# Performance work log

Hardware: AMD Instinct MI355X
Metric: run time of the kernel (lower is better)

## Reference

```python
import jax, jax.numpy as jnp
from jax import lax
import numpy as np

N_HEADS = 8
TANH_CLIP = 10.0
NEG = -1e9  # grad-safe stand-in for -inf mask value


def setup_inputs() -> dict:
    key = jax.random.key(0)
    k0, k1, k2, k3, k4 = jax.random.split(key, 5)
    B, N, D = 256, 512, 128
    s = 1.0 / np.sqrt(D)
    embeddings = jax.random.normal(k0, (B, N, D), jnp.float32)
    W_node = jax.random.normal(k1, (D, 3 * D), jnp.float32) * s   # project_node_embeddings
    W_fixed = jax.random.normal(k2, (D, D), jnp.float32) * s      # project_fixed_context
    W_step = jax.random.normal(k3, (D + 1, D), jnp.float32) * s   # project_step_context (D+1 input)
    W_out = jax.random.normal(k4, (D, D), jnp.float32) * s        # project_out
    return {"embeddings": embeddings, "W_node": W_node, "W_fixed": W_fixed,
            "W_step": W_step, "W_out": W_out, "num_steps": 64}


def reference(embeddings, W_node, W_fixed, W_step, W_out, num_steps):
    B, N, D = embeddings.shape
    H = N_HEADS
    dk = D // H
    dt = embeddings.dtype

    # ---- _precompute: fixed context, cached per-head keys/values, logit key ----
    graph_embed = embeddings.mean(axis=1)                     # [B, D]
    fixed_ctx = graph_embed @ W_fixed                         # [B, D]
    proj = embeddings @ W_node                                # [B, N, 3D]
    gK, gV, logitK = jnp.split(proj, 3, axis=-1)              # each [B, N, D]
    Kh = gK.reshape(B, N, H, dk).transpose(2, 0, 1, 3)        # [H, B, N, dk]
    Vh = gV.reshape(B, N, H, dk).transpose(2, 0, 1, 3)        # [H, B, N, dk]

    inv_sqrt_dk = jnp.asarray(1.0 / np.sqrt(dk), dt)
    inv_sqrt_d = jnp.asarray(1.0 / np.sqrt(D), dt)
    fracs = jnp.arange(num_steps, dtype=dt) / num_steps       # step-context scalar feature
    batch_idx = jnp.arange(B)

    def step(carry, frac):
        visited, current = carry                              # [B, N] bool, [B] int32
        # step context: current node embedding + scalar (remaining-fraction analogue)
        cur_emb = jnp.take_along_axis(embeddings, current[:, None, None], axis=1)[:, 0, :]
        step_ctx = jnp.concatenate([cur_emb, jnp.full((B, 1), frac, dt)], axis=-1)
        q = fixed_ctx + step_ctx @ W_step                     # [B, D] glimpse query
        Qh = q.reshape(B, H, dk).transpose(1, 0, 2)           # [H, B, dk]
        # glimpse attention with inner masking
        compat = jnp.einsum('hbd,hbnd->hbn', Qh, Kh) * inv_sqrt_dk
        compat = jnp.where(visited[None, :, :], NEG, compat)  # mask_inner
        attn = jax.nn.softmax(compat, axis=-1)
        heads = jnp.einsum('hbn,hbnd->hbd', attn, Vh)         # [H, B, dk]
        glimpse = heads.transpose(1, 0, 2).reshape(B, D) @ W_out
        # single-head tanh-clipped logits against logit key
        logits = jnp.einsum('bd,bnd->bn', glimpse, logitK) * inv_sqrt_d
        logits = jnp.tanh(logits) * TANH_CLIP
        logits = jnp.where(visited, NEG, logits)              # mask_logits
        log_p = jax.nn.log_softmax(logits, axis=-1)           # [B, N]
        selected = jnp.argmax(log_p, axis=-1).astype(jnp.int32)  # greedy decode
        visited = visited.at[batch_idx, selected].set(True)
        return (visited, selected), (log_p, selected)

    visited0 = jnp.zeros((B, N), bool)
    current0 = jnp.zeros((B,), jnp.int32)
    _, (log_ps, seqs) = lax.scan(step, (visited0, current0), fracs)
    return log_ps.transpose(1, 0, 2), seqs.transpose(1, 0)   # [B, T, N], [B, T]
```

## Files before the change

### kernel.cpp

```cpp
#include <hip/hip_runtime.h>

#define BB 256
#define NN 512
#define DD 128
#define HH 8

static constexpr float NEGC = -1e9f;
static constexpr float INV_SQRT_D = 0.08838834764831845f;

__device__ __forceinline__ float dot4(float4 a, float4 b) {
    return a.x * b.x + a.y * b.y + a.z * b.z + a.w * b.w;
}
__device__ __forceinline__ void fma4(float4& a, float p, float4 e) {
    a.x += p * e.x; a.y += p * e.y; a.z += p * e.z; a.w += p * e.w;
}

__global__ __launch_bounds__(128)
void precompute_fc(const float* __restrict__ E, const float* __restrict__ Wf,
                   float* __restrict__ fc) {
    int b = blockIdx.x, d = threadIdx.x;
    __shared__ float ge[DD];
    const float* Eb = E + (size_t)b * NN * DD;
    float s = 0.f;
    for (int n = 0; n < NN; ++n) s += Eb[n * DD + d];
    ge[d] = s * (1.0f / 512.0f);
    __syncthreads();
    float o = 0.f;
    for (int k = 0; k < DD; ++k) o += ge[k] * Wf[k * DD + d];
    fc[b * DD + d] = o;
}

__global__ __launch_bounds__(128)
void precompute_w(const float* __restrict__ Wn, const float* __restrict__ Wout,
                  float* __restrict__ Wog, float* __restrict__ WkT) {
    int k = blockIdx.x, d = threadIdx.x;
    WkT[k * DD + d] = Wn[d * 384 + k];
    float s = 0.f;
    for (int e = 0; e < DD; ++e) s += Wout[k * DD + e] * Wn[d * 384 + 256 + e];
    Wog[k * DD + d] = s;
}

struct SMw12 {
    float EA[NN * 64];
    float Pt[NN * 8];
    float qt[HH * DD];
    float qarr[DD];
    float fcs[DD];
    float hcv[DD];
    float gs[DD];
    float curE[DD];
    float l[HH];
    float Mh[HH];
    float redf[16];
    float stat[2];
    unsigned char visf[NN];
    int   cur;
    float rbv;
};

__global__ __launch_bounds__(512)
void decoder(const float* __restrict__ E, const float* __restrict__ Ws,
             const float* __restrict__ Wn, const float* __restrict__ fc,
             const float* __restrict__ Wog, const float* __restrict__ WkT,
             float* __restrict__ out_logp, float* __restrict__ out_seq, int T) {
    __shared__ SMw12 sm;
    const int b = blockIdx.x, tid = threadIdx.x;
    const int lane = tid & 63, wv = tid >> 6;
    const int g4 = tid >> 7, d128 = tid & 127;
    const float* Eg = E + (size_t)b * NN * DD;
    const float4* Ef4 = (const float4*)Eg;

    float* const slots = &sm.Pt[0];
    float* const part  = &sm.Pt[0];
    float* const lgp   = &sm.Pt[512];
    float* const ebp   = &sm.qt[0];

    #pragma unroll
    for (int i = 0; i < 16; ++i) {
        int f = i * 512 + tid;
        int nn = f >> 4, cq = f & 15;
        *(float4*)&sm.EA[nn * 64 + ((cq ^ (nn & 15)) << 2)] = Ef4[nn * 32 + cq];
    }
    if (tid < DD) {
        sm.fcs[tid] = fc[b * DD + tid];
        sm.curE[tid] = Eg[tid];
    }
    sm.visf[tid] = 0;
    if (tid == 0) sm.cur = 0;
    {
        float s = 0.f;
        #pragma unroll 8
        for (int i = 0; i < 32; ++i) { float4 v = Ef4[tid * 32 + i]; s += dot4(v, v); }
        for (int o = 1; o < 64; o <<= 1) s = fmaxf(s, __shfl_xor(s, o));
        if (lane == 0) sm.redf[wv] = s;
    }
    __syncthreads();
    if (tid == 0) {
        float m = sm.redf[0];
        for (int i = 1; i < 8; ++i) m = fmaxf(m, sm.redf[i]);
        sm.rbv = sqrtf(m);
    }
    __syncthreads();

    for (int t = 0; t < T; ++t) {
        {
            float s = 0.f;
            const float* Wsg = Ws + d128;
            int k0 = g4 * 32;
            #pragma unroll 8
            for (int k = k0; k < k0 + 32; ++k) s += sm.curE[k] * Wsg[k * DD];
            if (g4 == 3) s += ((float)t / (float)T) * Wsg[DD * DD];
            part[g4 * 128 + d128] = s;
        }
        __syncthreads();
        if (tid < DD)
            sm.qarr[tid] = sm.fcs[tid] + part[0 * 128 + tid] + part[1 * 128 + tid]
                         + part[2 * 128 + tid] + part[3 * 128 + tid];
        __syncthreads();
        {
            const int hA = g4, hB = g4 + 4;
            const float* WA = WkT + (hA * 16) * DD + d128;
            const float* WB = WkT + (hB * 16) * DD + d128;
            float a = 0.f, c = 0.f;
            #pragma unroll
            for (int j = 0; j < 16; ++j) {
                a += sm.qarr[hA * 16 + j] * WA[j * DD];
                c += sm.qarr[hB * 16 + j] * WB[j * DD];
            }
            a *= 0.25f; c *= 0.25f;
            sm.qt[hA * DD + d128] = a;
            sm.qt[hB * DD + d128] = c;
            float sa = a * a, sc = c * c;
            for (int o = 1; o < 64; o <<= 1) {
                sa += __shfl_xor(sa, o);
                sc += __shfl_xor(sc, o);
            }
            if (lane == 0) { sm.redf[wv] = sa; sm.redf[8 + wv] = sc; }
        }
        __syncthreads();
        if (tid < 8) {
            int h = tid;
            float ss = (h < 4) ? (sm.redf[2 * h] + sm.redf[2 * h + 1])
                               : (sm.redf[8 + 2 * (h - 4)] + sm.redf[8 + 2 * (h - 4) + 1]);
            sm.Mh[h] = sqrtf(ss) * sm.rbv;
        }
        __syncthreads();

        if (tid < 256) {
            const int n0 = tid, n1 = tid + 256;
            const int m0 = n0 & 15, m1 = n1 & 15;
            float b0 = 0.f, b1 = 0.f, b2 = 0.f, b3 = 0.f,
                  b4 = 0.f, b5 = 0.f, b6 = 0.f, b7 = 0.f;
            float c0 = 0.f, c1 = 0.f, c2 = 0.f, c3 = 0.f,
                  c4 = 0.f, c5 = 0.f, c6 = 0.f, c7 = 0.f;
            #pragma unroll 4
            for (int qd = 0; qd < 16; ++qd) {
                float4 e0 = *(const float4*)&sm.EA[n0 * 64 + ((qd ^ m0) << 2)];
                float4 e1 = *(const float4*)&sm.EA[n1 * 64 + ((qd ^ m1) << 2)];
#define CH(h_, bb_, cc_) { float4 qv = *(const float4*)&sm.qt[h_ * DD + qd * 4]; \
                bb_ += dot4(qv, e0); cc_ += dot4(qv, e1); }
                CH(0, b0, c0) CH(1, b1, c1) CH(2, b2, c2) CH(3, b3, c3)
                CH(4, b4, c4) CH(5, b5, c5) CH(6, b6, c6) CH(7, b7, c7)
#undef CH
            }
            #pragma unroll 4
            for (int qd = 0; qd < 16; ++qd) {
                float4 e0 = Ef4[n0 * 32 + 16 + qd];
                float4 e1 = Ef4[n1 * 32 + 16 + qd];
#define CH(h_, bb_, cc_) { float4 qv = *(const float4*)&sm.qt[h_ * DD + 64 + qd * 4]; \
                bb_ += dot4(qv, e0); cc_ += dot4(qv, e1); }
                CH(0, b0, c0) CH(1, b1, c1) CH(2, b2, c2) CH(3, b3, c3)
                CH(4, b4, c4) CH(5, b5, c5) CH(6, b6, c6) CH(7, b7, c7)
#undef CH
            }
            const bool v0 = (sm.visf[n0] != 0), v1 = (sm.visf[n1] != 0);
            float4 P0a, P0b, P1a, P1b;
            P0a.x = v0 ? 0.f : expf(b0 - sm.Mh[0]);
            P0a.y = v0 ? 0.f : expf(b1 - sm.Mh[1]);
            P0a.z = v0 ? 0.f : expf(b2 - sm.Mh[2]);
            P0a.w = v0 ? 0.f : expf(b3 - sm.Mh[3]);
            P0b.x = v0 ? 0.f : expf(b4 - sm.Mh[4]);
            P0b.y = v0 ? 0.f : expf(b5 - sm.Mh[5]);
            P0b.z = v0 ? 0.f : expf(b6 - sm.Mh[6]);
            P0b.w = v0 ? 0.f : expf(b7 - sm.Mh[7]);
            P1a.x = v1 ? 0.f : expf(c0 - sm.Mh[0]);
            P1a.y = v1 ? 0.f : expf(c1 - sm.Mh[1]);
            P1a.z = v1 ? 0.f : expf(c2 - sm.Mh[2]);
            P1a.w = v1 ? 0.f : expf(c3 - sm.Mh[3]);
            P1b.x = v1 ? 0.f : expf(c4 - sm.Mh[4]);
            P1b.y = v1 ? 0.f : expf(c5 - sm.Mh[5]);
            P1b.z = v1 ? 0.f : expf(c6 - sm.Mh[6]);
            P1b.w = v1 ? 0.f : expf(c7 - sm.Mh[7]);
            *(float4*)&sm.Pt[n0 * 8]     = P0a;
            *(float4*)&sm.Pt[n0 * 8 + 4] = P0b;
            *(float4*)&sm.Pt[n1 * 8]     = P1a;
            *(float4*)&sm.Pt[n1 * 8 + 4] = P1b;
        }
        __syncthreads();

        {
            const int h = wv;
            float sl = 0.f;
            #pragma unroll
            for (int i = 0; i < 8; ++i) sl += sm.Pt[(lane + i * 64) * 8 + h];
            for (int o = 1; o < 64; o <<= 1) sl += __shfl_xor(sl, o);
            if (lane == 0) sm.l[h] = sl;
        }
        const int dq = tid & 31, ch = tid >> 5;
        float4 a0 = {0,0,0,0}, a1 = {0,0,0,0}, a2 = {0,0,0,0}, a3 = {0,0,0,0},
               a4 = {0,0,0,0}, a5 = {0,0,0,0}, a6 = {0,0,0,0}, a7 = {0,0,0,0};
        {
            const int r0 = ch * 32;
            #pragma unroll 2
            for (int i = 0; i < 32; ++i) {
                const int r = r0 + i;
                float4 ev = (dq < 16)
                    ? *(const float4*)&sm.EA[r * 64 + ((dq ^ (r & 15)) << 2)]
                    : Ef4[r * 32 + dq];
                float4 pA = *(const float4*)&sm.Pt[r * 8];
                float4 pB = *(const float4*)&sm.Pt[r * 8 + 4];
                fma4(a0, pA.x, ev); fma4(a1, pA.y, ev);
                fma4(a2, pA.z, ev); fma4(a3, pA.w, ev);
                fma4(a4, pB.x, ev); fma4(a5, pB.y, ev);
                fma4(a6, pB.z, ev); fma4(a7, pB.w, ev);
            }
        }
        __syncthreads();
        {
            const int slot = ch & 3, rnd = ch >> 2;
            #pragma unroll
            for (int rr = 0; rr < 4; ++rr) {
                if (rnd == rr) {
                    float* sp = slots + (size_t)slot * 1024 + dq * 4;
                    if (rr == 0) {
#define STW(h_, av_) *(float4*)&sp[h_ * 128] = av_;
                        STW(0, a0) STW(1, a1) STW(2, a2) STW(3, a3)
                        STW(4, a4) STW(5, a5) STW(6, a6) STW(7, a7)
#undef STW
                    } else {
#define STA(h_, av_) { float4 tv = *(float4*)&sp[h_ * 128];                  \
                        tv.x += av_.x; tv.y += av_.y; tv.z += av_.z; tv.w += av_.w; \
                        *(float4*)&sp[h_ * 128] = tv; }
                        STA(0, a0) STA(1, a1) STA(2, a2) STA(3, a3)
                        STA(4, a4) STA(5, a5) STA(6, a6) STA(7, a7)
#undef STA
                    }
                }
                __syncthreads();
            }
        }
        {
            const int h = tid >> 6, d2 = (tid & 63) * 2;
            float inv = 1.0f / sm.l[h];
            #pragma unroll
            for (int r = 0; r < 2; ++r) {
                int d = d2 + r;
                float a = slots[0 * 1024 + h * 128 + d] + slots[1 * 1024 + h * 128 + d]
                        + slots[2 * 1024 + h * 128 + d] + slots[3 * 1024 + h * 128 + d];
                ebp[h * 128 + d] = a * inv;
            }
        }
        __syncthreads();

        {
            float s = 0.f;
            int k0 = g4 * 32;
            const int hh = d128 >> 4;
            const float* Wv = Wn + 128 + d128;
            #pragma unroll 8
            for (int d = k0; d < k0 + 32; ++d) s += ebp[hh * 128 + d] * Wv[d * 384];
            part[g4 * 128 + d128] = s;
        }
        __syncthreads();
        if (tid < DD)
            sm.hcv[tid] = part[0 * 128 + tid] + part[1 * 128 + tid]
                        + part[2 * 128 + tid] + part[3 * 128 + tid];
        __syncthreads();
        {
            float s = 0.f;
            int k0 = g4 * 32;
            #pragma unroll 8
            for (int k = k0; k < k0 + 32; ++k) s += sm.hcv[k] * Wog[k * DD + d128];
            part[g4 * 128 + d128] = s;
        }
        __syncthreads();
        if (tid < DD)
            sm.gs[tid] = (part[0 * 128 + tid] + part[1 * 128 + tid]
                        + part[2 * 128 + tid] + part[3 * 128 + tid]) * INV_SQRT_D;
        __syncthreads();

        {
            const int n = tid, nm = n & 15;
            float s = 0.f;
            #pragma unroll 4
            for (int qd = 0; qd < 16; ++qd) {
                float4 gq = *(const float4*)&sm.gs[qd * 4];
                float4 ev = *(const float4*)&sm.EA[n * 64 + ((qd ^ nm) << 2)];
                s += dot4(gq, ev);
            }
            #pragma unroll 4
            for (int qd = 0; qd < 16; ++qd) {
                float4 gq = *(const float4*)&sm.gs[64 + qd * 4];
                float4 ev = Ef4[n * 32 + 16 + qd];
                s += dot4(gq, ev);
            }
            lgp[n] = sm.visf[n] ? NEGC : 10.0f * tanhf(s);
        }
        __syncthreads();

        if (wv == 0) {
            float x0 = lgp[lane],       x1 = lgp[lane + 64],
                  x2 = lgp[lane + 128], x3 = lgp[lane + 192],
                  x4 = lgp[lane + 256], x5 = lgp[lane + 320],
                  x6 = lgp[lane + 384], x7 = lgp[lane + 448];
            float m = fmaxf(fmaxf(fmaxf(x0, x1), fmaxf(x2, x3)),
                            fmaxf(fmaxf(x4, x5), fmaxf(x6, x7)));
            for (int o = 1; o < 64; o <<= 1) m = fmaxf(m, __shfl_xor(m, o));
            float ssum = expf(x0 - m) + expf(x1 - m) + expf(x2 - m) + expf(x3 - m)
                       + expf(x4 - m) + expf(x5 - m) + expf(x6 - m) + expf(x7 - m);
            for (int o = 1; o < 64; o <<= 1) ssum += __shfl_xor(ssum, o);
            float lse = logf(ssum);
            float bv = (x0 - m) - lse; int bi = lane;
#define AMX(xi, ii) { float v_ = ((xi) - m) - lse; int i_ = (ii);           \
            if (v_ > bv) { bv = v_; bi = i_; } }
            AMX(x1, lane + 64)  AMX(x2, lane + 128) AMX(x3, lane + 192)
            AMX(x4, lane + 256) AMX(x5, lane + 320) AMX(x6, lane + 384)
            AMX(x7, lane + 448)
#undef AMX
            for (int o = 1; o < 64; o <<= 1) {
                float ov = __shfl_xor(bv, o);
                int   oi = __shfl_xor(bi, o);
                if (ov > bv || (ov == bv && oi < bi)) { bv = ov; bi = oi; }
            }
            if (lane == 0) {
                sm.stat[0] = m;
                sm.stat[1] = lse;
                sm.cur = bi;
                out_seq[(size_t)b * T + t] = (float)bi;
            }
        }
        __syncthreads();
        {
            float lp = (lgp[tid] - sm.stat[0]) - sm.stat[1];
            out_logp[((size_t)b * T + t) * NN + tid] = lp;
            const int cu = sm.cur;
            if (tid == cu) sm.visf[tid] = 1;
            if (tid < DD) {
                float vv;
                if (tid < 64)
                    vv = sm.EA[cu * 64 + ((((tid >> 2) ^ (cu & 15))) << 2) + (tid & 3)];
                else
                    vv = Eg[cu * DD + tid];
                sm.curE[tid] = vv;
            }
        }
        __syncthreads();
    }
}

extern "C" void kernel_launch(void* const* d_in, const int* in_sizes, int n_in,
                              void* d_out, int out_size, void* d_ws, size_t ws_size,
                              hipStream_t stream) {
    const float* E    = (const float*)d_in[0];
    const float* Wn   = (const float*)d_in[1];
    const float* Wf   = (const float*)d_in[2];
    const float* Ws   = (const float*)d_in[3];
    const float* Wout = (const float*)d_in[4];
    float* out = (float*)d_out;

    const int T = out_size / (BB * (NN + 1));

    float* fcp = (float*)d_ws;
    float* Wog = fcp + BB * DD;
    float* WkT = Wog + DD * DD;

    precompute_fc<<<BB, 128, 0, stream>>>(E, Wf, fcp);
    precompute_w<<<DD, 128, 0, stream>>>(Wn, Wout, Wog, WkT);
    decoder<<<BB, 512, 0, stream>>>(E, Ws, Wn, fcp, Wog, WkT,
                                    out, out + (size_t)BB * T * NN, T);
}
```

Baseline: 2.056 ms.

## Double decoder block to 1024 threads, splitting per-node dot products across thread pairs

Launches the decoder with 1024 threads per batch row instead of 512. The glimpse compat and logit dot products now split each node's 128-dim work across two threads (shared-memory half and global half), combined with a lane shuffle. The attention-value accumulation splits heads across half-waves so each thread holds 4 instead of 8 float4 accumulators. This aims to hide latency through more waves per block and lower register pressure, at the cost of padding the probability buffer and leaving half the threads idle in the small projection phases.

```diff
diff --git a/kernel.cpp b/kernel.cpp
--- a/kernel.cpp
+++ b/kernel.cpp
@@ -40,9 +40,9 @@
     Wog[k * DD + d] = s;
 }
 
-struct SMw12 {
+struct SMw15 {
     float EA[NN * 64];
-    float Pt[NN * 8];
+    float Pt[NN * 12];
     float qt[HH * DD];
     float qarr[DD];
     float fcs[DD];
@@ -58,26 +58,25 @@
     float rbv;
 };
 
-__global__ __launch_bounds__(512)
+__global__ __launch_bounds__(1024)
 void decoder(const float* __restrict__ E, const float* __restrict__ Ws,
              const float* __restrict__ Wn, const float* __restrict__ fc,
              const float* __restrict__ Wog, const float* __restrict__ WkT,
              float* __restrict__ out_logp, float* __restrict__ out_seq, int T) {
-    __shared__ SMw12 sm;
+    __shared__ SMw15 sm;
     const int b = blockIdx.x, tid = threadIdx.x;
     const int lane = tid & 63, wv = tid >> 6;
-    const int g4 = tid >> 7, d128 = tid & 127;
     const float* Eg = E + (size_t)b * NN * DD;
     const float4* Ef4 = (const float4*)Eg;
 
     float* const slots = &sm.Pt[0];
     float* const part  = &sm.Pt[0];
-    float* const lgp   = &sm.Pt[512];
+    float* const lgp   = &sm.Pt[4096];
     float* const ebp   = &sm.qt[0];
 
     #pragma unroll
-    for (int i = 0; i < 16; ++i) {
-        int f = i * 512 + tid;
+    for (int i = 0; i < 8; ++i) {
+        int f = i * 1024 + tid;
         int nn = f >> 4, cq = f & 15;
         *(float4*)&sm.EA[nn * 64 + ((cq ^ (nn & 15)) << 2)] = Ef4[nn * 32 + cq];
     }
@@ -85,9 +84,9 @@
         sm.fcs[tid] = fc[b * DD + tid];
         sm.curE[tid] = Eg[tid];
     }
-    sm.visf[tid] = 0;
+    if (tid < NN) sm.visf[tid] = 0;
     if (tid == 0) sm.cur = 0;
-    {
+    if (tid < NN) {
         float s = 0.f;
         #pragma unroll 8
         for (int i = 0; i < 32; ++i) { float4 v = Ef4[tid * 32 + i]; s += dot4(v, v); }
@@ -103,7 +102,8 @@
     __syncthreads();
 
     for (int t = 0; t < T; ++t) {
-        {
+        if (tid < 512) {
+            const int g4 = tid >> 7, d128 = tid & 127;
             float s = 0.f;
             const float* Wsg = Ws + d128;
             int k0 = g4 * 32;
@@ -117,7 +117,8 @@
             sm.qarr[tid] = sm.fcs[tid] + part[0 * 128 + tid] + part[1 * 128 + tid]
                          + part[2 * 128 + tid] + part[3 * 128 + tid];
         __syncthreads();
-        {
+        if (tid < 512) {
+            const int g4 = tid >> 7, d128 = tid & 127;
             const int hA = g4, hB = g4 + 4;
             const float* WA = WkT + (hA * 16) * DD + d128;
             const float* WB = WkT + (hB * 16) * DD + d128;
@@ -146,103 +147,98 @@
         }
         __syncthreads();
 
-        if (tid < 256) {
-            const int n0 = tid, n1 = tid + 256;
-            const int m0 = n0 & 15, m1 = n1 & 15;
-            float b0 = 0.f, b1 = 0.f, b2 = 0.f, b3 = 0.f,
-                  b4 = 0.f, b5 = 0.f, b6 = 0.f, b7 = 0.f;
-            float c0 = 0.f, c1 = 0.f, c2 = 0.f, c3 = 0.f,
-                  c4 = 0.f, c5 = 0.f, c6 = 0.f, c7 = 0.f;
-            #pragma unroll 4
-            for (int qd = 0; qd < 16; ++qd) {
-                float4 e0 = *(const float4*)&sm.EA[n0 * 64 + ((qd ^ m0) << 2)];
-                float4 e1 = *(const float4*)&sm.EA[n1 * 64 + ((qd ^ m1) << 2)];
-#define CH(h_, bb_, cc_) { float4 qv = *(const float4*)&sm.qt[h_ * DD + qd * 4]; \
-                bb_ += dot4(qv, e0); cc_ += dot4(qv, e1); }
-                CH(0, b0, c0) CH(1, b1, c1) CH(2, b2, c2) CH(3, b3, c3)
-                CH(4, b4, c4) CH(5, b5, c5) CH(6, b6, c6) CH(7, b7, c7)
-#undef CH
-            }
-            #pragma unroll 4
-            for (int qd = 0; qd < 16; ++qd) {
-                float4 e0 = Ef4[n0 * 32 + 16 + qd];
-                float4 e1 = Ef4[n1 * 32 + 16 + qd];
-#define CH(h_, bb_, cc_) { float4 qv = *(const float4*)&sm.qt[h_ * DD + 64 + qd * 4]; \
-                bb_ += dot4(qv, e0); cc_ += dot4(qv, e1); }
-                CH(0, b0, c0) CH(1, b1, c1) CH(2, b2, c2) CH(3, b3, c3)
-                CH(4, b4, c4) CH(5, b5, c5) CH(6, b6, c6) CH(7, b7, c7)
-#undef CH
-            }
-            const bool v0 = (sm.visf[n0] != 0), v1 = (sm.visf[n1] != 0);
-            float4 P0a, P0b, P1a, P1b;
-            P0a.x = v0 ? 0.f : expf(b0 - sm.Mh[0]);
-            P0a.y = v0 ? 0.f : expf(b1 - sm.Mh[1]);
-            P0a.z = v0 ? 0.f : expf(b2 - sm.Mh[2]);
-            P0a.w = v0 ? 0.f : expf(b3 - sm.Mh[3]);
-            P0b.x = v0 ? 0.f : expf(b4 - sm.Mh[4]);
-            P0b.y = v0 ? 0.f : expf(b5 - sm.Mh[5]);
-            P0b.z = v0 ? 0.f : expf(b6 - sm.Mh[6]);
-            P0b.w = v0 ? 0.f : expf(b7 - sm.Mh[7]);
-            P1a.x = v1 ? 0.f : expf(c0 - sm.Mh[0]);
-            P1a.y = v1 ? 0.f : expf(c1 - sm.Mh[1]);
-            P1a.z = v1 ? 0.f : expf(c2 - sm.Mh[2]);
-            P1a.w = v1 ? 0.f : expf(c3 - sm.Mh[3]);
-            P1b.x = v1 ? 0.f : expf(c4 - sm.Mh[4]);
-            P1b.y = v1 ? 0.f : expf(c5 - sm.Mh[5]);
-            P1b.z = v1 ? 0.f : expf(c6 - sm.Mh[6]);
-            P1b.w = v1 ? 0.f : expf(c7 - sm.Mh[7]);
-            *(float4*)&sm.Pt[n0 * 8]     = P0a;
-            *(float4*)&sm.Pt[n0 * 8 + 4] = P0b;
-            *(float4*)&sm.Pt[n1 * 8]     = P1a;
-            *(float4*)&sm.Pt[n1 * 8 + 4] = P1b;
-        }
-        __syncthreads();
-
         {
+            const int n2 = tid >> 1, hf = tid & 1;
+            float a0 = 0.f, a1 = 0.f, a2 = 0.f, a3 = 0.f,
+                  a4 = 0.f, a5 = 0.f, a6 = 0.f, a7 = 0.f;
+            if (hf == 0) {
+                const int nm = n2 & 15;
+                #pragma unroll 4
+                for (int q = 0; q < 16; ++q) {
+                    float4 ev = *(const float4*)&sm.EA[n2 * 64 + ((q ^ nm) << 2)];
+                    const int qb = q * 4;
+                    a0 += dot4(*(const float4*)&sm.qt[0 * DD + qb], ev);
+                    a1 += dot4(*(const float4*)&sm.qt[1 * DD + qb], ev);
+                    a2 += dot4(*(const float4*)&sm.qt[2 * DD + qb], ev);
+                    a3 += dot4(*(const float4*)&sm.qt[3 * DD + qb], ev);
+                    a4 += dot4(*(const float4*)&sm.qt[4 * DD + qb], ev);
+                    a5 += dot4(*(const float4*)&sm.qt[5 * DD + qb], ev);
+                    a6 += dot4(*(const float4*)&sm.qt[6 * DD + qb], ev);
+                    a7 += dot4(*(const float4*)&sm.qt[7 * DD + qb], ev);
+                }
+            } else {
+                #pragma unroll 4
+                for (int q = 0; q < 16; ++q) {
+                    float4 ev = Ef4[n2 * 32 + 16 + q];
+                    const int qb = 64 + q * 4;
+                    a0 += dot4(*(const float4*)&sm.qt[0 * DD + qb], ev);
+                    a1 += dot4(*(const float4*)&sm.qt[1 * DD + qb], ev);
+                    a2 += dot4(*(const float4*)&sm.qt[2 * DD + qb], ev);
+                    a3 += dot4(*(const float4*)&sm.qt[3 * DD + qb], ev);
+                    a4 += dot4(*(const float4*)&sm.qt[4 * DD + qb], ev);
+                    a5 += dot4(*(const float4*)&sm.qt[5 * DD + qb], ev);
+                    a6 += dot4(*(const float4*)&sm.qt[6 * DD + qb], ev);
+                    a7 += dot4(*(const float4*)&sm.qt[7 * DD + qb], ev);
+                }
+            }
+            a0 += __shfl_xor(a0, 1); a1 += __shfl_xor(a1, 1);
+            a2 += __shfl_xor(a2, 1); a3 += __shfl_xor(a3, 1);
+            a4 += __shfl_xor(a4, 1); a5 += __shfl_xor(a5, 1);
+            a6 += __shfl_xor(a6, 1); a7 += __shfl_xor(a7, 1);
+            if (hf == 0) {
+                const bool vn = (sm.visf[n2] != 0);
+                float4 Pa, Pb;
+                Pa.x = vn ? 0.f : expf(a0 - sm.Mh[0]);
+                Pa.y = vn ? 0.f : expf(a1 - sm.Mh[1]);
+                Pa.z = vn ? 0.f : expf(a2 - sm.Mh[2]);
+                Pa.w = vn ? 0.f : expf(a3 - sm.Mh[3]);
+                Pb.x = vn ? 0.f : expf(a4 - sm.Mh[4]);
+                Pb.y = vn ? 0.f : expf(a5 - sm.Mh[5]);
+                Pb.z = vn ? 0.f : expf(a6 - sm.Mh[6]);
+                Pb.w = vn ? 0.f : expf(a7 - sm.Mh[7]);
+                *(float4*)&sm.Pt[n2 * 12]     = Pa;
+                *(float4*)&sm.Pt[n2 * 12 + 4] = Pb;
+            }
+        }
+        __syncthreads();
+
+        if (wv < 8) {
             const int h = wv;
             float sl = 0.f;
             #pragma unroll
-            for (int i = 0; i < 8; ++i) sl += sm.Pt[(lane + i * 64) * 8 + h];
+            for (int i = 0; i < 8; ++i) sl += sm.Pt[(lane + i * 64) * 12 + h];
             for (int o = 1; o < 64; o <<= 1) sl += __shfl_xor(sl, o);
             if (lane == 0) sm.l[h] = sl;
         }
-        const int dq = tid & 31, ch = tid >> 5;
-        float4 a0 = {0,0,0,0}, a1 = {0,0,0,0}, a2 = {0,0,0,0}, a3 = {0,0,0,0},
-               a4 = {0,0,0,0}, a5 = {0,0,0,0}, a6 = {0,0,0,0}, a7 = {0,0,0,0};
         {
+            const int ch = wv, dq = lane & 31, hg = lane >> 5;
             const int r0 = ch * 32;
+            float4 a0 = {0,0,0,0}, a1 = {0,0,0,0}, a2 = {0,0,0,0}, a3 = {0,0,0,0};
             #pragma unroll 2
             for (int i = 0; i < 32; ++i) {
                 const int r = r0 + i;
                 float4 ev = (dq < 16)
                     ? *(const float4*)&sm.EA[r * 64 + ((dq ^ (r & 15)) << 2)]
                     : Ef4[r * 32 + dq];
-                float4 pA = *(const float4*)&sm.Pt[r * 8];
-                float4 pB = *(const float4*)&sm.Pt[r * 8 + 4];
-                fma4(a0, pA.x, ev); fma4(a1, pA.y, ev);
-                fma4(a2, pA.z, ev); fma4(a3, pA.w, ev);
-                fma4(a4, pB.x, ev); fma4(a5, pB.y, ev);
-                fma4(a6, pB.z, ev); fma4(a7, pB.w, ev);
-            }
-        }
-        __syncthreads();
-        {
+                float4 p = (hg == 0) ? *(const float4*)&sm.Pt[r * 12]
+                                     : *(const float4*)&sm.Pt[r * 12 + 4];
+                fma4(a0, p.x, ev); fma4(a1, p.y, ev);
+                fma4(a2, p.z, ev); fma4(a3, p.w, ev);
+            }
+            __syncthreads();
             const int slot = ch & 3, rnd = ch >> 2;
             #pragma unroll
             for (int rr = 0; rr < 4; ++rr) {
                 if (rnd == rr) {
-                    float* sp = slots + (size_t)slot * 1024 + dq * 4;
+                    float* sp = slots + (size_t)slot * 1024 + (size_t)hg * 512 + dq * 4;
                     if (rr == 0) {
-#define STW(h_, av_) *(float4*)&sp[h_ * 128] = av_;
-                        STW(0, a0) STW(1, a1) STW(2, a2) STW(3, a3)
-                        STW(4, a4) STW(5, a5) STW(6, a6) STW(7, a7)
-#undef STW
+                        *(float4*)&sp[0 * 128] = a0; *(float4*)&sp[1 * 128] = a1;
+                        *(float4*)&sp[2 * 128] = a2; *(float4*)&sp[3 * 128] = a3;
                     } else {
-#define STA(h_, av_) { float4 tv = *(float4*)&sp[h_ * 128];                  \
+#define STA(j_, av_) { float4 tv = *(float4*)&sp[j_ * 128];                      \
                         tv.x += av_.x; tv.y += av_.y; tv.z += av_.z; tv.w += av_.w; \
-                        *(float4*)&sp[h_ * 128] = tv; }
+                        *(float4*)&sp[j_ * 128] = tv; }
                         STA(0, a0) STA(1, a1) STA(2, a2) STA(3, a3)
-                        STA(4, a4) STA(5, a5) STA(6, a6) STA(7, a7)
 #undef STA
                     }
                 }
@@ -250,19 +246,15 @@
             }
         }
         {
-            const int h = tid >> 6, d2 = (tid & 63) * 2;
-            float inv = 1.0f / sm.l[h];
-            #pragma unroll
-            for (int r = 0; r < 2; ++r) {
-                int d = d2 + r;
-                float a = slots[0 * 1024 + h * 128 + d] + slots[1 * 1024 + h * 128 + d]
-                        + slots[2 * 1024 + h * 128 + d] + slots[3 * 1024 + h * 128 + d];
-                ebp[h * 128 + d] = a * inv;
-            }
-        }
-        __syncthreads();
-
-        {
+            const int h = tid >> 7, d = tid & 127;
+            float a = slots[0 * 1024 + h * 128 + d] + slots[1 * 1024 + h * 128 + d]
+                    + slots[2 * 1024 + h * 128 + d] + slots[3 * 1024 + h * 128 + d];
+            ebp[h * 128 + d] = a * (1.0f / sm.l[h]);
+        }
+        __syncthreads();
+
+        if (tid < 512) {
+            const int g4 = tid >> 7, d128 = tid & 127;
             float s = 0.f;
             int k0 = g4 * 32;
             const int hh = d128 >> 4;
@@ -276,7 +268,8 @@
             sm.hcv[tid] = part[0 * 128 + tid] + part[1 * 128 + tid]
                         + part[2 * 128 + tid] + part[3 * 128 + tid];
         __syncthreads();
-        {
+        if (tid < 512) {
+            const int g4 = tid >> 7, d128 = tid & 127;
             float s = 0.f;
             int k0 = g4 * 32;
             #pragma unroll 8
@@ -290,21 +283,24 @@
         __syncthreads();
 
         {
-            const int n = tid, nm = n & 15;
+            const int n2 = tid >> 1, hf = tid & 1;
             float s = 0.f;
-            #pragma unroll 4
-            for (int qd = 0; qd < 16; ++qd) {
-                float4 gq = *(const float4*)&sm.gs[qd * 4];
-                float4 ev = *(const float4*)&sm.EA[n * 64 + ((qd ^ nm) << 2)];
-                s += dot4(gq, ev);
-            }
-            #pragma unroll 4
-            for (int qd = 0; qd < 16; ++qd) {
-                float4 gq = *(const float4*)&sm.gs[64 + qd * 4];
-                float4 ev = Ef4[n * 32 + 16 + qd];
-                s += dot4(gq, ev);
-            }
-            lgp[n] = sm.visf[n] ? NEGC : 10.0f * tanhf(s);
+            if (hf == 0) {
+                const int nm = n2 & 15;
+                #pragma unroll 4
+                for (int q = 0; q < 16; ++q) {
+                    float4 ev = *(const float4*)&sm.EA[n2 * 64 + ((q ^ nm) << 2)];
+                    s += dot4(*(const float4*)&sm.gs[q * 4], ev);
+                }
+            } else {
+                #pragma unroll 4
+                for (int q = 0; q < 16; ++q) {
+                    float4 ev = Ef4[n2 * 32 + 16 + q];
+                    s += dot4(*(const float4*)&sm.gs[64 + q * 4], ev);
+                }
+            }
+            s += __shfl_xor(s, 1);
+            if (hf == 0) lgp[n2] = sm.visf[n2] ? NEGC : 10.0f * tanhf(s);
         }
         __syncthreads();
 
@@ -340,7 +336,7 @@
             }
         }
         __syncthreads();
-        {
+        if (tid < NN) {
             float lp = (lgp[tid] - sm.stat[0]) - sm.stat[1];
             out_logp[((size_t)b * T + t) * NN + tid] = lp;
             const int cu = sm.cur;
@@ -376,6 +372,6 @@
 
     precompute_fc<<<BB, 128, 0, stream>>>(E, Wf, fcp);
     precompute_w<<<DD, 128, 0, stream>>>(Wn, Wout, Wog, WkT);
-    decoder<<<BB, 512, 0, stream>>>(E, Ws, Wn, fcp, Wog, WkT,
-                                    out, out + (size_t)BB * T * NN, T);
-}
+    decoder<<<BB, 1024, 0, stream>>>(E, Ws, Wn, fcp, Wog, WkT,
+                                     out, out + (size_t)BB * T * NN, T);
+}
```

Result: slower. 4.131 ms (+101.0%).

## Fold value projection into output weights and drop per-step curE staging

Applied to the files above, without the earlier changes.

Precomputes per-head fused matrices Wvog (Wv_h · W_out · W_logitK) so each decode step does one matvec from the attention-weighted embeddings straight to the glimpse key vector. This removes a matvec, a reduction stage and two barriers per step. The step context now reads the current node embedding directly from global memory, which drops the curE shared buffer and the final barrier. The Pt stride is padded from 8 to 12 to cut LDS bank conflicts. The trade-off is a larger weight stream (8×128×128 floats) read every step.

```diff
diff --git a/kernel.cpp b/kernel.cpp
--- a/kernel.cpp
+++ b/kernel.cpp
@@ -40,15 +40,27 @@
     Wog[k * DD + d] = s;
 }
 
-struct SMw12 {
+__global__ __launch_bounds__(128)
+void precompute_w2(const float* __restrict__ Wn, const float* __restrict__ Wog,
+                   float* __restrict__ Wvog) {
+    int e = blockIdx.x, g = threadIdx.x;
+    #pragma unroll
+    for (int h = 0; h < 8; ++h) {
+        float s = 0.f;
+        #pragma unroll
+        for (int j = 0; j < 16; ++j)
+            s += Wn[e * 384 + 128 + 16 * h + j] * Wog[(16 * h + j) * 128 + g];
+        Wvog[((size_t)h * 128 + e) * 128 + g] = s;
+    }
+}
+
+struct SMw16 {
     float EA[NN * 64];
-    float Pt[NN * 8];
+    float Pt[NN * 12];
     float qt[HH * DD];
     float qarr[DD];
     float fcs[DD];
-    float hcv[DD];
     float gs[DD];
-    float curE[DD];
     float l[HH];
     float Mh[HH];
     float redf[16];
@@ -62,8 +74,9 @@
 void decoder(const float* __restrict__ E, const float* __restrict__ Ws,
              const float* __restrict__ Wn, const float* __restrict__ fc,
              const float* __restrict__ Wog, const float* __restrict__ WkT,
+             const float* __restrict__ Wvog,
              float* __restrict__ out_logp, float* __restrict__ out_seq, int T) {
-    __shared__ SMw12 sm;
+    __shared__ SMw16 sm;
     const int b = blockIdx.x, tid = threadIdx.x;
     const int lane = tid & 63, wv = tid >> 6;
     const int g4 = tid >> 7, d128 = tid & 127;
@@ -72,7 +85,7 @@
 
     float* const slots = &sm.Pt[0];
     float* const part  = &sm.Pt[0];
-    float* const lgp   = &sm.Pt[512];
+    float* const lgp   = &sm.Pt[4096];
     float* const ebp   = &sm.qt[0];
 
     #pragma unroll
@@ -81,10 +94,7 @@
         int nn = f >> 4, cq = f & 15;
         *(float4*)&sm.EA[nn * 64 + ((cq ^ (nn & 15)) << 2)] = Ef4[nn * 32 + cq];
     }
-    if (tid < DD) {
-        sm.fcs[tid] = fc[b * DD + tid];
-        sm.curE[tid] = Eg[tid];
-    }
+    if (tid < DD) sm.fcs[tid] = fc[b * DD + tid];
     sm.visf[tid] = 0;
     if (tid == 0) sm.cur = 0;
     {
@@ -104,11 +114,13 @@
 
     for (int t = 0; t < T; ++t) {
         {
+            const int cu = sm.cur;
+            const float* Ecur = Eg + (size_t)cu * DD;
+            const float* Wsg = Ws + d128;
             float s = 0.f;
-            const float* Wsg = Ws + d128;
             int k0 = g4 * 32;
             #pragma unroll 8
-            for (int k = k0; k < k0 + 32; ++k) s += sm.curE[k] * Wsg[k * DD];
+            for (int k = k0; k < k0 + 32; ++k) s += Ecur[k] * Wsg[k * DD];
             if (g4 == 3) s += ((float)t / (float)T) * Wsg[DD * DD];
             part[g4 * 128 + d128] = s;
         }
@@ -191,10 +203,10 @@
             P1b.y = v1 ? 0.f : expf(c5 - sm.Mh[5]);
             P1b.z = v1 ? 0.f : expf(c6 - sm.Mh[6]);
             P1b.w = v1 ? 0.f : expf(c7 - sm.Mh[7]);
-            *(float4*)&sm.Pt[n0 * 8]     = P0a;
-            *(float4*)&sm.Pt[n0 * 8 + 4] = P0b;
-            *(float4*)&sm.Pt[n1 * 8]     = P1a;
-            *(float4*)&sm.Pt[n1 * 8 + 4] = P1b;
+            *(float4*)&sm.Pt[n0 * 12]     = P0a;
+            *(float4*)&sm.Pt[n0 * 12 + 4] = P0b;
+            *(float4*)&sm.Pt[n1 * 12]     = P1a;
+            *(float4*)&sm.Pt[n1 * 12 + 4] = P1b;
         }
         __syncthreads();
 
@@ -202,7 +214,7 @@
             const int h = wv;
             float sl = 0.f;
             #pragma unroll
-            for (int i = 0; i < 8; ++i) sl += sm.Pt[(lane + i * 64) * 8 + h];
+            for (int i = 0; i < 8; ++i) sl += sm.Pt[(lane + i * 64) * 12 + h];
             for (int o = 1; o < 64; o <<= 1) sl += __shfl_xor(sl, o);
             if (lane == 0) sm.l[h] = sl;
         }
@@ -217,8 +229,8 @@
                 float4 ev = (dq < 16)
                     ? *(const float4*)&sm.EA[r * 64 + ((dq ^ (r & 15)) << 2)]
                     : Ef4[r * 32 + dq];
-                float4 pA = *(const float4*)&sm.Pt[r * 8];
-                float4 pB = *(const float4*)&sm.Pt[r * 8 + 4];
+                float4 pA = *(const float4*)&sm.Pt[r * 12];
+                float4 pB = *(const float4*)&sm.Pt[r * 12 + 4];
                 fma4(a0, pA.x, ev); fma4(a1, pA.y, ev);
                 fma4(a2, pA.z, ev); fma4(a3, pA.w, ev);
                 fma4(a4, pB.x, ev); fma4(a5, pB.y, ev);
@@ -263,24 +275,22 @@
         __syncthreads();
 
         {
+            const int h0 = g4 * 2;
+            const float* W0 = Wvog + ((size_t)h0 * 128) * 128 + d128;
+            const float* W1 = W0 + 128 * 128;
             float s = 0.f;
-            int k0 = g4 * 32;
-            const int hh = d128 >> 4;
-            const float* Wv = Wn + 128 + d128;
-            #pragma unroll 8
-            for (int d = k0; d < k0 + 32; ++d) s += ebp[hh * 128 + d] * Wv[d * 384];
-            part[g4 * 128 + d128] = s;
-        }
-        __syncthreads();
-        if (tid < DD)
-            sm.hcv[tid] = part[0 * 128 + tid] + part[1 * 128 + tid]
-                        + part[2 * 128 + tid] + part[3 * 128 + tid];
-        __syncthreads();
-        {
-            float s = 0.f;
-            int k0 = g4 * 32;
-            #pragma unroll 8
-            for (int k = k0; k < k0 + 32; ++k) s += sm.hcv[k] * Wog[k * DD + d128];
+            #pragma unroll 4
+            for (int eq = 0; eq < 32; ++eq) {
+                float4 e0 = *(const float4*)&ebp[h0 * 128 + eq * 4];
+                s += e0.x * W0[(eq * 4 + 0) * 128] + e0.y * W0[(eq * 4 + 1) * 128]
+                   + e0.z * W0[(eq * 4 + 2) * 128] + e0.w * W0[(eq * 4 + 3) * 128];
+            }
+            #pragma unroll 4
+            for (int eq = 0; eq < 32; ++eq) {
+                float4 e1 = *(const float4*)&ebp[(h0 + 1) * 128 + eq * 4];
+                s += e1.x * W1[(eq * 4 + 0) * 128] + e1.y * W1[(eq * 4 + 1) * 128]
+                   + e1.z * W1[(eq * 4 + 2) * 128] + e1.w * W1[(eq * 4 + 3) * 128];
+            }
             part[g4 * 128 + d128] = s;
         }
         __syncthreads();
@@ -343,18 +353,8 @@
         {
             float lp = (lgp[tid] - sm.stat[0]) - sm.stat[1];
             out_logp[((size_t)b * T + t) * NN + tid] = lp;
-            const int cu = sm.cur;
-            if (tid == cu) sm.visf[tid] = 1;
-            if (tid < DD) {
-                float vv;
-                if (tid < 64)
-                    vv = sm.EA[cu * 64 + ((((tid >> 2) ^ (cu & 15))) << 2) + (tid & 3)];
-                else
-                    vv = Eg[cu * DD + tid];
-                sm.curE[tid] = vv;
-            }
-        }
-        __syncthreads();
+            if (tid == sm.cur) sm.visf[tid] = 1;
+        }
     }
 }
 
@@ -370,12 +370,14 @@
 
     const int T = out_size / (BB * (NN + 1));
 
-    float* fcp = (float*)d_ws;
-    float* Wog = fcp + BB * DD;
-    float* WkT = Wog + DD * DD;
+    float* fcp  = (float*)d_ws;
+    float* Wog  = fcp + BB * DD;
+    float* WkT  = Wog + DD * DD;
+    float* Wvog = WkT + DD * DD;
 
     precompute_fc<<<BB, 128, 0, stream>>>(E, Wf, fcp);
     precompute_w<<<DD, 128, 0, stream>>>(Wn, Wout, Wog, WkT);
-    decoder<<<BB, 512, 0, stream>>>(E, Ws, Wn, fcp, Wog, WkT,
+    precompute_w2<<<DD, 128, 0, stream>>>(Wn, Wog, Wvog);
+    decoder<<<BB, 512, 0, stream>>>(E, Ws, Wn, fcp, Wog, WkT, Wvog,
                                     out, out + (size_t)BB * T * NN, T);
 }
```

Result: slower. 2.230 ms (+8.5%).

## Eliminate block barriers by redundant per-thread reductions and per-wave argmax

Applied to the files above, without the earlier changes.

Removes several __syncthreads per decode step. Small reduction stages (qarr, Mh, hcv, gs) are folded into their consumers, which re-sum the partial buffers redundantly. Every wave now computes the log-softmax and argmax itself, so the current node is held in a register and no broadcast barrier is needed. The Pt stride grows to 12 to make room for a second partial buffer. The cost is redundant shared-memory reads and arithmetic per thread, plus extra LDS usage.

```diff
diff --git a/kernel.cpp b/kernel.cpp
--- a/kernel.cpp
+++ b/kernel.cpp
@@ -40,21 +40,14 @@
     Wog[k * DD + d] = s;
 }
 
-struct SMw12 {
+struct SMw17 {
     float EA[NN * 64];
-    float Pt[NN * 8];
+    float Pt[NN * 12];
     float qt[HH * DD];
-    float qarr[DD];
     float fcs[DD];
-    float hcv[DD];
-    float gs[DD];
-    float curE[DD];
+    float redf[16];
     float l[HH];
-    float Mh[HH];
-    float redf[16];
-    float stat[2];
     unsigned char visf[NN];
-    int   cur;
     float rbv;
 };
 
@@ -63,7 +56,7 @@
              const float* __restrict__ Wn, const float* __restrict__ fc,
              const float* __restrict__ Wog, const float* __restrict__ WkT,
              float* __restrict__ out_logp, float* __restrict__ out_seq, int T) {
-    __shared__ SMw12 sm;
+    __shared__ SMw17 sm;
     const int b = blockIdx.x, tid = threadIdx.x;
     const int lane = tid & 63, wv = tid >> 6;
     const int g4 = tid >> 7, d128 = tid & 127;
@@ -72,7 +65,8 @@
 
     float* const slots = &sm.Pt[0];
     float* const part  = &sm.Pt[0];
-    float* const lgp   = &sm.Pt[512];
+    float* const part2 = &sm.Pt[512];
+    float* const lgp   = &sm.Pt[4096];
     float* const ebp   = &sm.qt[0];
 
     #pragma unroll
@@ -81,12 +75,9 @@
         int nn = f >> 4, cq = f & 15;
         *(float4*)&sm.EA[nn * 64 + ((cq ^ (nn & 15)) << 2)] = Ef4[nn * 32 + cq];
     }
-    if (tid < DD) {
-        sm.fcs[tid] = fc[b * DD + tid];
-        sm.curE[tid] = Eg[tid];
-    }
+    if (tid < DD) sm.fcs[tid] = fc[b * DD + tid];
     sm.visf[tid] = 0;
-    if (tid == 0) sm.cur = 0;
+    int cur = 0;
     {
         float s = 0.f;
         #pragma unroll 8
@@ -104,18 +95,15 @@
 
     for (int t = 0; t < T; ++t) {
         {
+            const float* Ecur = Eg + (size_t)cur * DD;
+            const float* Wsg = Ws + d128;
             float s = 0.f;
-            const float* Wsg = Ws + d128;
             int k0 = g4 * 32;
             #pragma unroll 8
-            for (int k = k0; k < k0 + 32; ++k) s += sm.curE[k] * Wsg[k * DD];
+            for (int k = k0; k < k0 + 32; ++k) s += Ecur[k] * Wsg[k * DD];
             if (g4 == 3) s += ((float)t / (float)T) * Wsg[DD * DD];
             part[g4 * 128 + d128] = s;
         }
-        __syncthreads();
-        if (tid < DD)
-            sm.qarr[tid] = sm.fcs[tid] + part[0 * 128 + tid] + part[1 * 128 + tid]
-                         + part[2 * 128 + tid] + part[3 * 128 + tid];
         __syncthreads();
         {
             const int hA = g4, hB = g4 + 4;
@@ -124,8 +112,13 @@
             float a = 0.f, c = 0.f;
             #pragma unroll
             for (int j = 0; j < 16; ++j) {
-                a += sm.qarr[hA * 16 + j] * WA[j * DD];
-                c += sm.qarr[hB * 16 + j] * WB[j * DD];
+                const int iA = hA * 16 + j, iB = hB * 16 + j;
+                float qA = sm.fcs[iA] + part[0 * 128 + iA] + part[1 * 128 + iA]
+                         + part[2 * 128 + iA] + part[3 * 128 + iA];
+                float qB = sm.fcs[iB] + part[0 * 128 + iB] + part[1 * 128 + iB]
+                         + part[2 * 128 + iB] + part[3 * 128 + iB];
+                a += qA * WA[j * DD];
+                c += qB * WB[j * DD];
             }
             a *= 0.25f; c *= 0.25f;
             sm.qt[hA * DD + d128] = a;
@@ -138,15 +131,16 @@
             if (lane == 0) { sm.redf[wv] = sa; sm.redf[8 + wv] = sc; }
         }
         __syncthreads();
-        if (tid < 8) {
-            int h = tid;
-            float ss = (h < 4) ? (sm.redf[2 * h] + sm.redf[2 * h + 1])
-                               : (sm.redf[8 + 2 * (h - 4)] + sm.redf[8 + 2 * (h - 4) + 1]);
-            sm.Mh[h] = sqrtf(ss) * sm.rbv;
-        }
-        __syncthreads();
-
         if (tid < 256) {
+            const float rb = sm.rbv;
+            float mh0 = sqrtf(sm.redf[0]  + sm.redf[1])  * rb;
+            float mh1 = sqrtf(sm.redf[2]  + sm.redf[3])  * rb;
+            float mh2 = sqrtf(sm.redf[4]  + sm.redf[5])  * rb;
+            float mh3 = sqrtf(sm.redf[6]  + sm.redf[7])  * rb;
+            float mh4 = sqrtf(sm.redf[8]  + sm.redf[9])  * rb;
+            float mh5 = sqrtf(sm.redf[10] + sm.redf[11]) * rb;
+            float mh6 = sqrtf(sm.redf[12] + sm.redf[13]) * rb;
+            float mh7 = sqrtf(sm.redf[14] + sm.redf[15]) * rb;
             const int n0 = tid, n1 = tid + 256;
             const int m0 = n0 & 15, m1 = n1 & 15;
             float b0 = 0.f, b1 = 0.f, b2 = 0.f, b3 = 0.f,
@@ -175,26 +169,26 @@
             }
             const bool v0 = (sm.visf[n0] != 0), v1 = (sm.visf[n1] != 0);
             float4 P0a, P0b, P1a, P1b;
-            P0a.x = v0 ? 0.f : expf(b0 - sm.Mh[0]);
-            P0a.y = v0 ? 0.f : expf(b1 - sm.Mh[1]);
-            P0a.z = v0 ? 0.f : expf(b2 - sm.Mh[2]);
-            P0a.w = v0 ? 0.f : expf(b3 - sm.Mh[3]);
-            P0b.x = v0 ? 0.f : expf(b4 - sm.Mh[4]);
-            P0b.y = v0 ? 0.f : expf(b5 - sm.Mh[5]);
-            P0b.z = v0 ? 0.f : expf(b6 - sm.Mh[6]);
-            P0b.w = v0 ? 0.f : expf(b7 - sm.Mh[7]);
-            P1a.x = v1 ? 0.f : expf(c0 - sm.Mh[0]);
-            P1a.y = v1 ? 0.f : expf(c1 - sm.Mh[1]);
-            P1a.z = v1 ? 0.f : expf(c2 - sm.Mh[2]);
-            P1a.w = v1 ? 0.f : expf(c3 - sm.Mh[3]);
-            P1b.x = v1 ? 0.f : expf(c4 - sm.Mh[4]);
-            P1b.y = v1 ? 0.f : expf(c5 - sm.Mh[5]);
-            P1b.z = v1 ? 0.f : expf(c6 - sm.Mh[6]);
-            P1b.w = v1 ? 0.f : expf(c7 - sm.Mh[7]);
-            *(float4*)&sm.Pt[n0 * 8]     = P0a;
-            *(float4*)&sm.Pt[n0 * 8 + 4] = P0b;
-            *(float4*)&sm.Pt[n1 * 8]     = P1a;
-            *(float4*)&sm.Pt[n1 * 8 + 4] = P1b;
+            P0a.x = v0 ? 0.f : expf(b0 - mh0);
+            P0a.y = v0 ? 0.f : expf(b1 - mh1);
+            P0a.z = v0 ? 0.f : expf(b2 - mh2);
+            P0a.w = v0 ? 0.f : expf(b3 - mh3);
+            P0b.x = v0 ? 0.f : expf(b4 - mh4);
+            P0b.y = v0 ? 0.f : expf(b5 - mh5);
+            P0b.z = v0 ? 0.f : expf(b6 - mh6);
+            P0b.w = v0 ? 0.f : expf(b7 - mh7);
+            P1a.x = v1 ? 0.f : expf(c0 - mh0);
+            P1a.y = v1 ? 0.f : expf(c1 - mh1);
+            P1a.z = v1 ? 0.f : expf(c2 - mh2);
+            P1a.w = v1 ? 0.f : expf(c3 - mh3);
+            P1b.x = v1 ? 0.f : expf(c4 - mh4);
+            P1b.y = v1 ? 0.f : expf(c5 - mh5);
+            P1b.z = v1 ? 0.f : expf(c6 - mh6);
+            P1b.w = v1 ? 0.f : expf(c7 - mh7);
+            *(float4*)&sm.Pt[n0 * 12]     = P0a;
+            *(float4*)&sm.Pt[n0 * 12 + 4] = P0b;
+            *(float4*)&sm.Pt[n1 * 12]     = P1a;
+            *(float4*)&sm.Pt[n1 * 12 + 4] = P1b;
         }
         __syncthreads();
 
@@ -202,7 +196,7 @@
             const int h = wv;
             float sl = 0.f;
             #pragma unroll
-            for (int i = 0; i < 8; ++i) sl += sm.Pt[(lane + i * 64) * 8 + h];
+            for (int i = 0; i < 8; ++i) sl += sm.Pt[(lane + i * 64) * 12 + h];
             for (int o = 1; o < 64; o <<= 1) sl += __shfl_xor(sl, o);
             if (lane == 0) sm.l[h] = sl;
         }
@@ -217,8 +211,8 @@
                 float4 ev = (dq < 16)
                     ? *(const float4*)&sm.EA[r * 64 + ((dq ^ (r & 15)) << 2)]
                     : Ef4[r * 32 + dq];
-                float4 pA = *(const float4*)&sm.Pt[r * 8];
-                float4 pB = *(const float4*)&sm.Pt[r * 8 + 4];
+                float4 pA = *(const float4*)&sm.Pt[r * 12];
+                float4 pB = *(const float4*)&sm.Pt[r * 12 + 4];
                 fma4(a0, pA.x, ev); fma4(a1, pA.y, ev);
                 fma4(a2, pA.z, ev); fma4(a3, pA.w, ev);
                 fma4(a4, pB.x, ev); fma4(a5, pB.y, ev);
@@ -272,35 +266,47 @@
             part[g4 * 128 + d128] = s;
         }
         __syncthreads();
-        if (tid < DD)
-            sm.hcv[tid] = part[0 * 128 + tid] + part[1 * 128 + tid]
-                        + part[2 * 128 + tid] + part[3 * 128 + tid];
-        __syncthreads();
         {
             float s = 0.f;
             int k0 = g4 * 32;
             #pragma unroll 8
-            for (int k = k0; k < k0 + 32; ++k) s += sm.hcv[k] * Wog[k * DD + d128];
-            part[g4 * 128 + d128] = s;
-        }
-        __syncthreads();
-        if (tid < DD)
-            sm.gs[tid] = (part[0 * 128 + tid] + part[1 * 128 + tid]
-                        + part[2 * 128 + tid] + part[3 * 128 + tid]) * INV_SQRT_D;
-        __syncthreads();
-
+            for (int k = k0; k < k0 + 32; ++k) {
+                float hck = part[0 * 128 + k] + part[1 * 128 + k]
+                          + part[2 * 128 + k] + part[3 * 128 + k];
+                s += hck * Wog[k * DD + d128];
+            }
+            part2[g4 * 128 + d128] = s;
+        }
+        __syncthreads();
         {
             const int n = tid, nm = n & 15;
             float s = 0.f;
             #pragma unroll 4
             for (int qd = 0; qd < 16; ++qd) {
-                float4 gq = *(const float4*)&sm.gs[qd * 4];
+                float4 p0 = *(const float4*)&part2[0 * 128 + qd * 4];
+                float4 p1 = *(const float4*)&part2[1 * 128 + qd * 4];
+                float4 p2 = *(const float4*)&part2[2 * 128 + qd * 4];
+                float4 p3 = *(const float4*)&part2[3 * 128 + qd * 4];
+                float4 gq;
+                gq.x = (p0.x + p1.x + p2.x + p3.x) * INV_SQRT_D;
+                gq.y = (p0.y + p1.y + p2.y + p3.y) * INV_SQRT_D;
+                gq.z = (p0.z + p1.z + p2.z + p3.z) * INV_SQRT_D;
+                gq.w = (p0.w + p1.w + p2.w + p3.w) * INV_SQRT_D;
                 float4 ev = *(const float4*)&sm.EA[n * 64 + ((qd ^ nm) << 2)];
                 s += dot4(gq, ev);
             }
             #pragma unroll 4
             for (int qd = 0; qd < 16; ++qd) {
-                float4 gq = *(const float4*)&sm.gs[64 + qd * 4];
+                const int i0 = 64 + qd * 4;
+                float4 p0 = *(const float4*)&part2[0 * 128 + i0];
+                float4 p1 = *(const float4*)&part2[1 * 128 + i0];
+                float4 p2 = *(const float4*)&part2[2 * 128 + i0];
+                float4 p3 = *(const float4*)&part2[3 * 128 + i0];
+                float4 gq;
+                gq.x = (p0.x + p1.x + p2.x + p3.x) * INV_SQRT_D;
+                gq.y = (p0.y + p1.y + p2.y + p3.y) * INV_SQRT_D;
+                gq.z = (p0.z + p1.z + p2.z + p3.z) * INV_SQRT_D;
+                gq.w = (p0.w + p1.w + p2.w + p3.w) * INV_SQRT_D;
                 float4 ev = Ef4[n * 32 + 16 + qd];
                 s += dot4(gq, ev);
             }
@@ -308,7 +314,7 @@
         }
         __syncthreads();
 
-        if (wv == 0) {
+        {
             float x0 = lgp[lane],       x1 = lgp[lane + 64],
                   x2 = lgp[lane + 128], x3 = lgp[lane + 192],
                   x4 = lgp[lane + 256], x5 = lgp[lane + 320],
@@ -332,29 +338,12 @@
                 int   oi = __shfl_xor(bi, o);
                 if (ov > bv || (ov == bv && oi < bi)) { bv = ov; bi = oi; }
             }
-            if (lane == 0) {
-                sm.stat[0] = m;
-                sm.stat[1] = lse;
-                sm.cur = bi;
-                out_seq[(size_t)b * T + t] = (float)bi;
-            }
-        }
-        __syncthreads();
-        {
-            float lp = (lgp[tid] - sm.stat[0]) - sm.stat[1];
+            cur = bi;
+            float lp = (lgp[tid] - m) - lse;
             out_logp[((size_t)b * T + t) * NN + tid] = lp;
-            const int cu = sm.cur;
-            if (tid == cu) sm.visf[tid] = 1;
-            if (tid < DD) {
-                float vv;
-                if (tid < 64)
-                    vv = sm.EA[cu * 64 + ((((tid >> 2) ^ (cu & 15))) << 2) + (tid & 3)];
-                else
-                    vv = Eg[cu * DD + tid];
-                sm.curE[tid] = vv;
-            }
-        }
-        __syncthreads();
+            if (wv == 0 && lane == 0) out_seq[(size_t)b * T + t] = (float)bi;
+            if (tid == cur) sm.visf[tid] = 1;
+        }
     }
 }
 
```

Result: slower. 2.212 ms (+7.6%).
